# Performance work log

Hardware: AMD Instinct MI355X
Metric: run time of the kernel (lower is better)

The kernel has to match this reference:

```python
import jax, jax.numpy as jnp
import numpy as np

N_NODES = 100000
N_EDGES = 800000
IN_FEATS = 128
HIDDEN = 128
NUM_CLASSES = 10
NUM_GRAPHS = 128
BN_EPS = 1e-5


def setup_inputs() -> dict:
    key = jax.random.key(0)
    ks = jax.random.split(key, 16)
    s = 0.05  # weight init scale
    return {
        "x": jax.random.normal(ks[0], (N_NODES, IN_FEATS), dtype=jnp.float32),
        "edge_index": jax.random.randint(ks[1], (2, N_EDGES), 0, N_NODES, dtype=jnp.int64),
        "batch": jnp.sort(jax.random.randint(ks[2], (N_NODES,), 0, NUM_GRAPHS, dtype=jnp.int64)),
        # conv1 MLP: Linear(in,h) -> ReLU -> Linear(h,h)
        "W1a": jax.random.normal(ks[3], (IN_FEATS, HIDDEN), dtype=jnp.float32) * s,
        "b1a": jnp.zeros((HIDDEN,), dtype=jnp.float32),
        "W1b": jax.random.normal(ks[4], (HIDDEN, HIDDEN), dtype=jnp.float32) * s,
        "b1b": jnp.zeros((HIDDEN,), dtype=jnp.float32),
        "gamma1": jnp.ones((HIDDEN,), dtype=jnp.float32),
        "beta1": jnp.zeros((HIDDEN,), dtype=jnp.float32),
        # conv2 MLP
        "W2a": jax.random.normal(ks[5], (HIDDEN, HIDDEN), dtype=jnp.float32) * s,
        "b2a": jnp.zeros((HIDDEN,), dtype=jnp.float32),
        "W2b": jax.random.normal(ks[6], (HIDDEN, HIDDEN), dtype=jnp.float32) * s,
        "b2b": jnp.zeros((HIDDEN,), dtype=jnp.float32),
        "gamma2": jnp.ones((HIDDEN,), dtype=jnp.float32),
        "beta2": jnp.zeros((HIDDEN,), dtype=jnp.float32),
        # final classifier
        "Wlin": jax.random.normal(ks[7], (HIDDEN, NUM_CLASSES), dtype=jnp.float32) * s,
        "blin": jnp.zeros((NUM_CLASSES,), dtype=jnp.float32),
    }


def _gin_conv(x, edge_index, Wa, ba, Wb, bb, eps=0.0):
    # GINConv: MLP((1+eps)*x_i + sum_{j->i} x_j); scatter-add over edges
    src, dst = edge_index[0], edge_index[1]
    agg = jax.ops.segment_sum(x[src], dst, num_segments=N_NODES)
    h = (1.0 + eps) * x + agg
    h = jax.nn.relu(h @ Wa + ba) @ Wb + bb
    return h


def _batch_norm(x, gamma, beta):
    # training-mode BN over the node dim (biased variance, as in torch)
    mean = jnp.mean(x, axis=0)
    var = jnp.mean(jnp.square(x - mean), axis=0)
    return (x - mean) * jax.lax.rsqrt(var + BN_EPS) * gamma + beta


def reference(x, edge_index, batch, W1a, b1a, W1b, b1b, gamma1, beta1,
              W2a, b2a, W2b, b2b, gamma2, beta2, Wlin, blin):
    h = _gin_conv(x, edge_index, W1a, b1a, W1b, b1b)
    h = jax.nn.relu(_batch_norm(h, gamma1, beta1))
    # dropout: eval mode -> identity
    h = _gin_conv(h, edge_index, W2a, b2a, W2b, b2b)
    h = jax.nn.relu(_batch_norm(h, gamma2, beta2))
    # global mean pool per graph
    summed = jax.ops.segment_sum(h, batch, num_segments=NUM_GRAPHS)
    counts = jax.ops.segment_sum(jnp.ones((h.shape[0],), h.dtype), batch, num_segments=NUM_GRAPHS)
    pooled = summed / jnp.maximum(counts, 1.0)[:, None]  # [G, H]
    logits = pooled @ Wlin + blin
    return jax.nn.log_softmax(logits, axis=1)
```

## Files before the change

kernel.cpp:

```cpp
#include <hip/hip_runtime.h>

#define N_NODES 100000
#define N_EDGESC 800000
#define HID 128
#define NGRAPH 128
#define BN_EPS 1e-5f
#define NREP 32
#define PS 136
#define MLP_BLOCKS ((N_NODES + 63) / 64)

#define PBLK 256
#define PCHUNK 3125
#define NCOARSE 196
#define HISTN (NCOARSE * PBLK)
#define HSCAN_BLOCKS (HISTN / 1024)
#define CVT_BLOCKS 12500

typedef __bf16 bf16x8 __attribute__((ext_vector_type(8)));
typedef float f32x4 __attribute__((ext_vector_type(4)));

__device__ inline unsigned short f2bf(float f) {
    unsigned int u = __float_as_uint(f);
    unsigned int r = u + 0x7FFFu + ((u >> 16) & 1u);
    return (unsigned short)(r >> 16);
}
__device__ inline float b2f(unsigned short u) {
    return __uint_as_float(((unsigned int)u) << 16);
}


__global__ __launch_bounds__(256) void k_phist(const int* __restrict__ dst,
                                               int* __restrict__ hist)
{
    __shared__ int h[NCOARSE];
    if (threadIdx.x < NCOARSE) h[threadIdx.x] = 0;
    __syncthreads();
    int base = blockIdx.x * PCHUNK;
    for (int i = threadIdx.x; i < PCHUNK; i += 256)
        atomicAdd(&h[dst[base + i] >> 9], 1);
    __syncthreads();
    if (threadIdx.x < NCOARSE)
        hist[threadIdx.x * PBLK + blockIdx.x] = h[threadIdx.x];
}

__global__ __launch_bounds__(256) void k_scan_block(int* __restrict__ a,
    int* __restrict__ bsum, int n)
{
    __shared__ int ts[256];
    int base = blockIdx.x * 1024 + threadIdx.x * 4;
    int v[4], s = 0;
    #pragma unroll
    for (int i = 0; i < 4; ++i) {
        int idx = base + i;
        v[i] = (idx < n) ? a[idx] : 0;
        s += v[i];
    }
    ts[threadIdx.x] = s;
    __syncthreads();
    for (int d = 1; d < 256; d <<= 1) {
        int t = (threadIdx.x >= d) ? ts[threadIdx.x - d] : 0;
        __syncthreads();
        ts[threadIdx.x] += t;
        __syncthreads();
    }
    int run = ts[threadIdx.x] - s;
    #pragma unroll
    for (int i = 0; i < 4; ++i) {
        int idx = base + i;
        if (idx < n) a[idx] = run;
        run += v[i];
    }
    if (threadIdx.x == 255) bsum[blockIdx.x] = ts[255];
}

__global__ void k_scan_top_bounds(int* __restrict__ bsum, int nb,
    const int* __restrict__ batch, int* __restrict__ gstart)
{
    if (threadIdx.x == 0) {
        int run = 0;
        for (int i = 0; i < nb; ++i) { int t = bsum[i]; bsum[i] = run; run += t; }
    }
    int g = threadIdx.x;
    int lo = 0, hi = N_NODES;
    while (lo < hi) {
        int mid = (lo + hi) >> 1;
        if (batch[mid] < g) lo = mid + 1; else hi = mid;
    }
    gstart[g] = lo;
    if (g == 0) gstart[NGRAPH] = N_NODES;
}

__global__ __launch_bounds__(256) void k_pscatter(const int* __restrict__ src,
    const int* __restrict__ dst, const int* __restrict__ hist,
    const int* __restrict__ bsum, unsigned int* __restrict__ pk1)
{
    __shared__ int cur[NCOARSE];
    if (threadIdx.x < NCOARSE) {
        int idx = threadIdx.x * PBLK + blockIdx.x;
        cur[threadIdx.x] = hist[idx] + bsum[idx >> 10];
    }
    __syncthreads();
    int base = blockIdx.x * PCHUNK;
    for (int i = threadIdx.x; i < PCHUNK; i += 256) {
        int s = src[base + i], d = dst[base + i];
        int p = atomicAdd(&cur[d >> 9], 1);
        pk1[p] = ((unsigned int)s << 9) | (unsigned int)(d & 511);
    }
}

__global__ __launch_bounds__(256) void k_psort(const unsigned int* __restrict__ pk1,
    const int* __restrict__ hist, const int* __restrict__ bsum,
    int* __restrict__ eidx, int* __restrict__ off)
{
    __shared__ int h[512], cur[512], ts[256];
    const int b = blockIdx.x;
    const int i0 = b * PBLK;
    const int e0 = hist[i0] + bsum[i0 >> 10];
    int e1 = N_EDGESC;
    if (b < NCOARSE - 1) {
        const int i1 = (b + 1) * PBLK;
        e1 = hist[i1] + bsum[i1 >> 10];
    }
    const int cnt = e1 - e0;
    h[threadIdx.x] = 0; h[threadIdx.x + 256] = 0;
    __syncthreads();
    for (int i = threadIdx.x; i < cnt; i += 256)
        atomicAdd(&h[pk1[e0 + i] & 511], 1);
    __syncthreads();
    int v0 = h[threadIdx.x * 2], v1 = h[threadIdx.x * 2 + 1];
    int s = v0 + v1;
    ts[threadIdx.x] = s;
    __syncthreads();
    for (int d = 1; d < 256; d <<= 1) {
        int t = (threadIdx.x >= d) ? ts[threadIdx.x - d] : 0;
        __syncthreads();
        ts[threadIdx.x] += t;
        __syncthreads();
    }
    int run = e0 + ts[threadIdx.x] - s;
    int n0 = b * 512 + threadIdx.x * 2;
    cur[threadIdx.x * 2]     = run;
    cur[threadIdx.x * 2 + 1] = run + v0;
    if (n0     <= N_NODES) off[n0]     = run;
    if (n0 + 1 <= N_NODES) off[n0 + 1] = run + v0;
    __syncthreads();
    for (int i = threadIdx.x; i < cnt; i += 256) {
        unsigned int u = pk1[e0 + i];
        int p = atomicAdd(&cur[u & 511], 1);
        eidx[p] = (int)(u >> 9);
    }
}

__global__ __launch_bounds__(256) void k_cvtw(const float* __restrict__ X,
    unsigned short* __restrict__ Y,
    const float* __restrict__ Wa, const float* __restrict__ Wb,
    const float* __restrict__ Wc, const float* __restrict__ Wd,
    unsigned short* __restrict__ WT)
{
    int blk = blockIdx.x;
    if (blk < CVT_BLOCKS) {
        int i = blk * 256 + threadIdx.x;
        float4 v = ((const float4*)X)[i];
        ((ushort4*)Y)[i] = make_ushort4(f2bf(v.x), f2bf(v.y), f2bf(v.z), f2bf(v.w));
    } else {
        int idx = (blk - CVT_BLOCKS) * 256 + threadIdx.x;
        int mat = idx >> 14, w = idx & 16383;
        int k = w >> 7, n = w & 127;
        const float* W = (mat == 0) ? Wa : (mat == 1) ? Wb : (mat == 2) ? Wc : Wd;
        WT[mat * 16384 + n * 128 + k] = f2bf(W[w]);
    }
}

template<bool BN>
__device__ inline void acc_row(float* acc, uint4 v,
                               const float* sc, const float* sh)
{
    unsigned int u[4] = {v.x, v.y, v.z, v.w};
    #pragma unroll
    for (int j = 0; j < 4; ++j) {
        float lo = b2f((unsigned short)u[j]);
        float hi = b2f((unsigned short)(u[j] >> 16));
        if (BN) {
            lo = fmaxf(lo * sc[2*j]   + sh[2*j],   0.f);
            hi = fmaxf(hi * sc[2*j+1] + sh[2*j+1], 0.f);
        }
        acc[2*j]   += lo;
        acc[2*j+1] += hi;
    }
}

template<bool BN>
__global__ __launch_bounds__(256) void k_gather(
    const unsigned short* __restrict__ X, const float* __restrict__ SC,
    const int* __restrict__ off, const int* __restrict__ eidx,
    unsigned short* __restrict__ OUT, int M)
{
    int n = blockIdx.x * 16 + (threadIdx.x >> 4);
    if (n >= M) return;
    const int lane = threadIdx.x & 15;
    const size_t co = (size_t)lane * 8;

    float sc[8], sh[8];
    if (BN) {
        *(float4*)&sc[0] = ((const float4*)SC)[lane * 2];
        *(float4*)&sc[4] = ((const float4*)SC)[lane * 2 + 1];
        *(float4*)&sh[0] = ((const float4*)SC)[32 + lane * 2];
        *(float4*)&sh[4] = ((const float4*)SC)[32 + lane * 2 + 1];
    }

    float acc[8] = {0.f, 0.f, 0.f, 0.f, 0.f, 0.f, 0.f, 0.f};
    acc_row<BN>(acc, *(const uint4*)(X + (size_t)n * HID + co), sc, sh);

    int k = off[n], kend = off[n + 1];
    for (; k + 7 < kend; k += 8) {
        uint4 v0 = *(const uint4*)(X + (size_t)eidx[k]   * HID + co);
        uint4 v1 = *(const uint4*)(X + (size_t)eidx[k+1] * HID + co);
        uint4 v2 = *(const uint4*)(X + (size_t)eidx[k+2] * HID + co);
        uint4 v3 = *(const uint4*)(X + (size_t)eidx[k+3] * HID + co);
        uint4 v4 = *(const uint4*)(X + (size_t)eidx[k+4] * HID + co);
        uint4 v5 = *(const uint4*)(X + (size_t)eidx[k+5] * HID + co);
        uint4 v6 = *(const uint4*)(X + (size_t)eidx[k+6] * HID + co);
        uint4 v7 = *(const uint4*)(X + (size_t)eidx[k+7] * HID + co);
        acc_row<BN>(acc, v0, sc, sh); acc_row<BN>(acc, v1, sc, sh);
        acc_row<BN>(acc, v2, sc, sh); acc_row<BN>(acc, v3, sc, sh);
        acc_row<BN>(acc, v4, sc, sh); acc_row<BN>(acc, v5, sc, sh);
        acc_row<BN>(acc, v6, sc, sh); acc_row<BN>(acc, v7, sc, sh);
    }
    for (; k + 3 < kend; k += 4) {
        uint4 v0 = *(const uint4*)(X + (size_t)eidx[k]   * HID + co);
        uint4 v1 = *(const uint4*)(X + (size_t)eidx[k+1] * HID + co);
        uint4 v2 = *(const uint4*)(X + (size_t)eidx[k+2] * HID + co);
        uint4 v3 = *(const uint4*)(X + (size_t)eidx[k+3] * HID + co);
        acc_row<BN>(acc, v0, sc, sh); acc_row<BN>(acc, v1, sc, sh);
        acc_row<BN>(acc, v2, sc, sh); acc_row<BN>(acc, v3, sc, sh);
    }
    for (; k < kend; ++k) {
        uint4 v = *(const uint4*)(X + (size_t)eidx[k] * HID + co);
        acc_row<BN>(acc, v, sc, sh);
    }

    uint4 o;
    o.x = (unsigned int)f2bf(acc[0]) | ((unsigned int)f2bf(acc[1]) << 16);
    o.y = (unsigned int)f2bf(acc[2]) | ((unsigned int)f2bf(acc[3]) << 16);
    o.z = (unsigned int)f2bf(acc[4]) | ((unsigned int)f2bf(acc[5]) << 16);
    o.w = (unsigned int)f2bf(acc[6]) | ((unsigned int)f2bf(acc[7]) << 16);
    *(uint4*)(OUT + (size_t)n * HID + co) = o;
}

__global__ __launch_bounds__(256) void k_mlp(
    const unsigned short* __restrict__ A,
    const unsigned short* __restrict__ WTa, const float* __restrict__ ba,
    const unsigned short* __restrict__ WTb, const float* __restrict__ bb,
    unsigned short* __restrict__ Cb, float* __restrict__ Srep, int M)
{
    __shared__ unsigned short Abuf[64 * PS];
    __shared__ unsigned short Hbuf[64 * PS];

    const int tid  = threadIdx.x;
    const int wave = tid >> 6;
    const int lane = tid & 63;
    const int m    = lane & 15;
    const int quad = lane >> 4;
    const int rowbase = blockIdx.x * 64;

    bf16x8 WA[2][4], WB[2][4];
    float bav[2], bbv[2];
    #pragma unroll
    for (int n0 = 0; n0 < 2; ++n0) {
        const int col = (wave * 2 + n0) * 16 + m;
        const size_t cb = (size_t)col * HID + quad * 8;
        #pragma unroll
        for (int kk = 0; kk < 4; ++kk) {
            WA[n0][kk] = *(const bf16x8*)(WTa + cb + kk * 32);
            WB[n0][kk] = *(const bf16x8*)(WTb + cb + kk * 32);
        }
        bav[n0] = ba[col];
        bbv[n0] = bb[col];
    }

    {
        const uint4* Ag = (const uint4*)(A + (size_t)rowbase * HID);
        #pragma unroll
        for (int i = 0; i < 4; ++i) {
            int u = tid + i * 256;
            uint4 v = Ag[u];
            int r = u >> 4, c = u & 15;
            *(uint4*)(Abuf + r * PS + c * 8) = v;
        }
    }
    __syncthreads();

    f32x4 acc[4][2];
    #pragma unroll
    for (int rg = 0; rg < 4; ++rg)
        #pragma unroll
        for (int n0 = 0; n0 < 2; ++n0) acc[rg][n0] = {0.f, 0.f, 0.f, 0.f};
    #pragma unroll
    for (int rg = 0; rg < 4; ++rg) {
        #pragma unroll
        for (int kk = 0; kk < 4; ++kk) {
            bf16x8 af = *(const bf16x8*)(Abuf + (rg*16 + m) * PS + quad*8 + kk*32);
            acc[rg][0] = __builtin_amdgcn_mfma_f32_16x16x32_bf16(af, WA[0][kk], acc[rg][0], 0, 0, 0);
            acc[rg][1] = __builtin_amdgcn_mfma_f32_16x16x32_bf16(af, WA[1][kk], acc[rg][1], 0, 0, 0);
        }
    }

    #pragma unroll
    for (int rg = 0; rg < 4; ++rg)
        #pragma unroll
        for (int n0 = 0; n0 < 2; ++n0)
            #pragma unroll
            for (int i = 0; i < 4; ++i)
                Hbuf[(rg*16 + quad*4 + i) * PS + (wave*2 + n0)*16 + m] =
                    f2bf(fmaxf(acc[rg][n0][i] + bav[n0], 0.f));
    __syncthreads();

    #pragma unroll
    for (int rg = 0; rg < 4; ++rg)
        #pragma unroll
        for (int n0 = 0; n0 < 2; ++n0) acc[rg][n0] = {0.f, 0.f, 0.f, 0.f};
    #pragma unroll
    for (int rg = 0; rg < 4; ++rg) {
        #pragma unroll
        for (int kk = 0; kk < 4; ++kk) {
            bf16x8 hf = *(const bf16x8*)(Hbuf + (rg*16 + m) * PS + quad*8 + kk*32);
            acc[rg][0] = __builtin_amdgcn_mfma_f32_16x16x32_bf16(hf, WB[0][kk], acc[rg][0], 0, 0, 0);
            acc[rg][1] = __builtin_amdgcn_mfma_f32_16x16x32_bf16(hf, WB[1][kk], acc[rg][1], 0, 0, 0);
        }
    }

    const bool full = (rowbase + 64 <= M);
    float s[2] = {0.f, 0.f}, s2[2] = {0.f, 0.f};
    #pragma unroll
    for (int rg = 0; rg < 4; ++rg) {
        #pragma unroll
        for (int n0 = 0; n0 < 2; ++n0) {
            #pragma unroll
            for (int i = 0; i < 4; ++i) {
                float v = acc[rg][n0][i] + bbv[n0];
                if (full || rowbase + rg*16 + quad*4 + i < M) { s[n0] += v; s2[n0] += v*v; }
                Abuf[(rg*16 + quad*4 + i) * PS + (wave*2 + n0)*16 + m] = f2bf(v);
            }
        }
    }
    __syncthreads();

    #pragma unroll
    for (int i = 0; i < 4; ++i) {
        int u = tid + i * 256;
        int r = u >> 4, c = u & 15;
        uint4 v = *(const uint4*)(Abuf + r * PS + c * 8);
        int g = rowbase + r;
        if (g < M) *(uint4*)(Cb + (size_t)g * HID + c * 8) = v;
    }

    #pragma unroll
    for (int n0 = 0; n0 < 2; ++n0) {
        s[n0]  += __shfl_xor(s[n0], 16, 64);
        s[n0]  += __shfl_xor(s[n0], 32, 64);
        s2[n0] += __shfl_xor(s2[n0], 16, 64);
        s2[n0] += __shfl_xor(s2[n0], 32, 64);
    }
    if (quad == 0) {
        float* R = Srep + (size_t)((blockIdx.x * 4 + wave) & (NREP - 1)) * 256;
        #pragma unroll
        for (int n0 = 0; n0 < 2; ++n0) {
            int col = (wave * 2 + n0) * 16 + m;
            atomicAdd(&R[col], s[n0]);
            atomicAdd(&R[128 + col], s2[n0]);
        }
    }
}

__global__ void k_bnfinalize(const float* __restrict__ Srep,
    const float* __restrict__ gamma, const float* __restrict__ beta,
    float* __restrict__ SC, int M)
{
    int f = threadIdx.x;
    float s = 0.f, s2 = 0.f;
    for (int r = 0; r < NREP; ++r) {
        s += Srep[r * 256 + f];
        s2 += Srep[r * 256 + 128 + f];
    }
    float mean = s / (float)M;
    float var = s2 / (float)M - mean * mean;
    var = fmaxf(var, 0.f);
    float sc = gamma[f] * rsqrtf(var + BN_EPS);
    SC[f] = sc;
    SC[HID + f] = beta[f] - mean * sc;
}

__global__ __launch_bounds__(256) void k_pool(const unsigned short* __restrict__ H,
    const float* __restrict__ SC, const int* __restrict__ gstart,
    float* __restrict__ P)
{
    int g = blockIdx.x >> 4, part = blockIdx.x & 15;
    int beg = gstart[g], end = gstart[g + 1];
    int f = threadIdx.x & 127, half = threadIdx.x >> 7;
    float sc = SC[f], sh = SC[HID + f];
    float s = 0.f;
    for (int r = beg + part * 2 + half; r < end; r += 32)
        s += fmaxf(b2f(H[(size_t)r * HID + f]) * sc + sh, 0.f);
    __shared__ float ls[256];
    ls[threadIdx.x] = s;
    __syncthreads();
    if (threadIdx.x < 128)
        atomicAdd(&P[g * HID + threadIdx.x], ls[threadIdx.x] + ls[threadIdx.x + 128]);
}

__global__ void k_head(const float* __restrict__ P, const int* __restrict__ gstart,
    const float* __restrict__ Wlin, const float* __restrict__ blin,
    float* __restrict__ out)
{
    int g = blockIdx.x;
    int l = threadIdx.x;
    float inv = 1.f / (float)max(gstart[g + 1] - gstart[g], 1);
    float p0 = P[(size_t)g * HID + l] * inv;
    float p1 = P[(size_t)g * HID + 64 + l] * inv;
    float lg[10];
    #pragma unroll
    for (int c = 0; c < 10; ++c) {
        float v = p0 * Wlin[l * 10 + c] + p1 * Wlin[(64 + l) * 10 + c];
        #pragma unroll
        for (int off = 32; off > 0; off >>= 1) v += __shfl_down(v, off);
        lg[c] = v;
    }
    if (l == 0) {
        float mx = -1e30f;
        #pragma unroll
        for (int c = 0; c < 10; ++c) { lg[c] += blin[c]; mx = fmaxf(mx, lg[c]); }
        float s = 0.f;
        #pragma unroll
        for (int c = 0; c < 10; ++c) s += expf(lg[c] - mx);
        float lse = mx + logf(s);
        #pragma unroll
        for (int c = 0; c < 10; ++c) out[g * 10 + c] = lg[c] - lse;
    }
}

extern "C" void kernel_launch(void* const* d_in, const int* in_sizes, int n_in,
                              void* d_out, int out_size, void* d_ws, size_t ws_size,
                              hipStream_t stream)
{
    const float* x    = (const float*)d_in[0];
    const int*   ei   = (const int*)d_in[1];
    const int*   batch= (const int*)d_in[2];
    const float* W1a  = (const float*)d_in[3];
    const float* b1a  = (const float*)d_in[4];
    const float* W1b  = (const float*)d_in[5];
    const float* b1b  = (const float*)d_in[6];
    const float* g1   = (const float*)d_in[7];
    const float* be1  = (const float*)d_in[8];
    const float* W2a  = (const float*)d_in[9];
    const float* b2a  = (const float*)d_in[10];
    const float* W2b  = (const float*)d_in[11];
    const float* b2b  = (const float*)d_in[12];
    const float* g2   = (const float*)d_in[13];
    const float* be2  = (const float*)d_in[14];
    const float* Wl   = (const float*)d_in[15];
    const float* bl   = (const float*)d_in[16];
    float* out = (float*)d_out;

    const int* src = ei;
    const int* dst = ei + N_EDGESC;

    const size_t NM = (size_t)N_NODES * HID;
    char* wsb = (char*)d_ws;
    unsigned short* Ab  = (unsigned short*)wsb;
    unsigned short* Yb  = Ab + NM;
    unsigned short* Xb  = Yb + NM;
    float* Srep1 = (float*)(Xb + NM);
    float* Srep2 = Srep1 + NREP * 256;
    float* P    = Srep2 + NREP * 256;
    float* SC1  = P + (size_t)NGRAPH * HID;
    float* SC2  = SC1 + 256;
    unsigned short* WT = (unsigned short*)(SC2 + 256);
    int* hist   = (int*)(WT + 4 * 16384);
    int* eidx   = hist + HISTN;
    int* off    = eidx + N_EDGESC;
    int* bsum   = off + N_NODES + 1;
    int* gstart = bsum + 64;
    unsigned int* pk1 = (unsigned int*)Xb;

    dim3 blk(256);
    const int gatBlocks = (N_NODES + 15) / 16;

    hipMemsetAsync(Srep1, 0,
        (2 * NREP * 256 + (size_t)NGRAPH * HID) * sizeof(float), stream);

    k_phist<<<PBLK, blk, 0, stream>>>(dst, hist);
    k_scan_block<<<HSCAN_BLOCKS, blk, 0, stream>>>(hist, bsum, HISTN);
    k_scan_top_bounds<<<1, 128, 0, stream>>>(bsum, HSCAN_BLOCKS, batch, gstart);
    k_pscatter<<<PBLK, blk, 0, stream>>>(src, dst, hist, bsum, pk1);
    k_psort<<<NCOARSE, blk, 0, stream>>>(pk1, hist, bsum, eidx, off);

    k_cvtw<<<CVT_BLOCKS + 256, blk, 0, stream>>>(x, Xb, W1a, W1b, W2a, W2b, WT);

    k_gather<false><<<gatBlocks, blk, 0, stream>>>(Xb, nullptr, off, eidx, Ab, N_NODES);
    k_mlp<<<MLP_BLOCKS, blk, 0, stream>>>(Ab, WT, b1a, WT + 16384, b1b, Yb, Srep1, N_NODES);
    k_bnfinalize<<<1, 128, 0, stream>>>(Srep1, g1, be1, SC1, N_NODES);

    k_gather<true><<<gatBlocks, blk, 0, stream>>>(Yb, SC1, off, eidx, Ab, N_NODES);
    k_mlp<<<MLP_BLOCKS, blk, 0, stream>>>(Ab, WT + 2 * 16384, b2a, WT + 3 * 16384, b2b, Xb, Srep2, N_NODES);
    k_bnfinalize<<<1, 128, 0, stream>>>(Srep2, g2, be2, SC2, N_NODES);

    k_pool<<<NGRAPH * 16, blk, 0, stream>>>(Xb, SC2, gstart, P);
    k_head<<<NGRAPH, 64, 0, stream>>>(P, gstart, Wl, bl, out);
}
```

Measured before the change: 302.9 us.

## Merge CSR prep into cooperative kernel, fold BN finalize and pooling into neighbors

Five edge-sort preprocessing kernels are merged into one cooperative kernel that uses grid-wide syncs between phases. BN finalize now runs in the last-finishing block of each MLP kernel, found with an atomic done-counter. Pool and head become one kernel with one block per graph. This removes several launches and the pooled-sum memset and atomics, but pooling now runs on only 128 blocks and grid.sync adds its own cost.

```diff
diff --git a/kernel.cpp b/kernel.cpp
--- a/kernel.cpp
+++ b/kernel.cpp
@@ -1,4 +1,7 @@
 #include <hip/hip_runtime.h>
+#include <hip/hip_cooperative_groups.h>
+
+namespace cg = cooperative_groups;
 
 #define N_NODES 100000
 #define N_EDGESC 800000
@@ -28,126 +31,121 @@
     return __uint_as_float(((unsigned int)u) << 16);
 }
 
-
-__global__ __launch_bounds__(256) void k_phist(const int* __restrict__ dst,
-                                               int* __restrict__ hist)
-{
-    __shared__ int h[NCOARSE];
-    if (threadIdx.x < NCOARSE) h[threadIdx.x] = 0;
-    __syncthreads();
-    int base = blockIdx.x * PCHUNK;
-    for (int i = threadIdx.x; i < PCHUNK; i += 256)
-        atomicAdd(&h[dst[base + i] >> 9], 1);
-    __syncthreads();
-    if (threadIdx.x < NCOARSE)
-        hist[threadIdx.x * PBLK + blockIdx.x] = h[threadIdx.x];
-}
-
-__global__ __launch_bounds__(256) void k_scan_block(int* __restrict__ a,
-    int* __restrict__ bsum, int n)
-{
-    __shared__ int ts[256];
-    int base = blockIdx.x * 1024 + threadIdx.x * 4;
-    int v[4], s = 0;
-    #pragma unroll
-    for (int i = 0; i < 4; ++i) {
-        int idx = base + i;
-        v[i] = (idx < n) ? a[idx] : 0;
-        s += v[i];
-    }
-    ts[threadIdx.x] = s;
-    __syncthreads();
-    for (int d = 1; d < 256; d <<= 1) {
-        int t = (threadIdx.x >= d) ? ts[threadIdx.x - d] : 0;
-        __syncthreads();
-        ts[threadIdx.x] += t;
-        __syncthreads();
-    }
-    int run = ts[threadIdx.x] - s;
-    #pragma unroll
-    for (int i = 0; i < 4; ++i) {
-        int idx = base + i;
-        if (idx < n) a[idx] = run;
-        run += v[i];
-    }
-    if (threadIdx.x == 255) bsum[blockIdx.x] = ts[255];
-}
-
-__global__ void k_scan_top_bounds(int* __restrict__ bsum, int nb,
-    const int* __restrict__ batch, int* __restrict__ gstart)
-{
-    if (threadIdx.x == 0) {
-        int run = 0;
-        for (int i = 0; i < nb; ++i) { int t = bsum[i]; bsum[i] = run; run += t; }
-    }
-    int g = threadIdx.x;
-    int lo = 0, hi = N_NODES;
-    while (lo < hi) {
-        int mid = (lo + hi) >> 1;
-        if (batch[mid] < g) lo = mid + 1; else hi = mid;
-    }
-    gstart[g] = lo;
-    if (g == 0) gstart[NGRAPH] = N_NODES;
-}
-
-__global__ __launch_bounds__(256) void k_pscatter(const int* __restrict__ src,
-    const int* __restrict__ dst, const int* __restrict__ hist,
-    const int* __restrict__ bsum, unsigned int* __restrict__ pk1)
-{
-    __shared__ int cur[NCOARSE];
-    if (threadIdx.x < NCOARSE) {
-        int idx = threadIdx.x * PBLK + blockIdx.x;
-        cur[threadIdx.x] = hist[idx] + bsum[idx >> 10];
-    }
-    __syncthreads();
-    int base = blockIdx.x * PCHUNK;
-    for (int i = threadIdx.x; i < PCHUNK; i += 256) {
-        int s = src[base + i], d = dst[base + i];
-        int p = atomicAdd(&cur[d >> 9], 1);
-        pk1[p] = ((unsigned int)s << 9) | (unsigned int)(d & 511);
-    }
-}
-
-__global__ __launch_bounds__(256) void k_psort(const unsigned int* __restrict__ pk1,
-    const int* __restrict__ hist, const int* __restrict__ bsum,
-    int* __restrict__ eidx, int* __restrict__ off)
-{
-    __shared__ int h[512], cur[512], ts[256];
+__global__ __launch_bounds__(256) void k_prep(
+    const int* __restrict__ src, const int* __restrict__ dst,
+    const int* __restrict__ batch,
+    int* __restrict__ hist, int* __restrict__ bsum, int* __restrict__ gstart,
+    unsigned int* __restrict__ pk1, int* __restrict__ eidx, int* __restrict__ off)
+{
+    cg::grid_group grid = cg::this_grid();
+    __shared__ int S[1280];
+    const int tid = threadIdx.x;
     const int b = blockIdx.x;
-    const int i0 = b * PBLK;
-    const int e0 = hist[i0] + bsum[i0 >> 10];
-    int e1 = N_EDGESC;
-    if (b < NCOARSE - 1) {
-        const int i1 = (b + 1) * PBLK;
-        e1 = hist[i1] + bsum[i1 >> 10];
-    }
-    const int cnt = e1 - e0;
-    h[threadIdx.x] = 0; h[threadIdx.x + 256] = 0;
-    __syncthreads();
-    for (int i = threadIdx.x; i < cnt; i += 256)
-        atomicAdd(&h[pk1[e0 + i] & 511], 1);
-    __syncthreads();
-    int v0 = h[threadIdx.x * 2], v1 = h[threadIdx.x * 2 + 1];
-    int s = v0 + v1;
-    ts[threadIdx.x] = s;
-    __syncthreads();
-    for (int d = 1; d < 256; d <<= 1) {
-        int t = (threadIdx.x >= d) ? ts[threadIdx.x - d] : 0;
-        __syncthreads();
-        ts[threadIdx.x] += t;
-        __syncthreads();
-    }
-    int run = e0 + ts[threadIdx.x] - s;
-    int n0 = b * 512 + threadIdx.x * 2;
-    cur[threadIdx.x * 2]     = run;
-    cur[threadIdx.x * 2 + 1] = run + v0;
-    if (n0     <= N_NODES) off[n0]     = run;
-    if (n0 + 1 <= N_NODES) off[n0 + 1] = run + v0;
-    __syncthreads();
-    for (int i = threadIdx.x; i < cnt; i += 256) {
-        unsigned int u = pk1[e0 + i];
-        int p = atomicAdd(&cur[u & 511], 1);
-        eidx[p] = (int)(u >> 9);
+
+    {
+        int* h = S;
+        if (tid < NCOARSE) h[tid] = 0;
+        __syncthreads();
+        int base = b * PCHUNK;
+        for (int i = tid; i < PCHUNK; i += 256)
+            atomicAdd(&h[dst[base + i] >> 9], 1);
+        __syncthreads();
+        if (tid < NCOARSE) hist[tid * PBLK + b] = h[tid];
+    }
+    grid.sync();
+
+    if (b < HSCAN_BLOCKS) {
+        int* ts = S;
+        int base = b * 1024 + tid * 4;
+        int v[4], s = 0;
+        #pragma unroll
+        for (int i = 0; i < 4; ++i) { v[i] = hist[base + i]; s += v[i]; }
+        ts[tid] = s;
+        __syncthreads();
+        for (int d = 1; d < 256; d <<= 1) {
+            int t = (tid >= d) ? ts[tid - d] : 0;
+            __syncthreads();
+            ts[tid] += t;
+            __syncthreads();
+        }
+        int run = ts[tid] - s;
+        #pragma unroll
+        for (int i = 0; i < 4; ++i) { hist[base + i] = run; run += v[i]; }
+        if (tid == 255) bsum[b] = ts[255];
+    }
+    grid.sync();
+
+    if (b == 0) {
+        if (tid == 0) {
+            int run = 0;
+            for (int i = 0; i < HSCAN_BLOCKS; ++i) { int t = bsum[i]; bsum[i] = run; run += t; }
+        }
+        if (tid < 128) {
+            int g = tid;
+            int lo = 0, hi = N_NODES;
+            while (lo < hi) {
+                int mid = (lo + hi) >> 1;
+                if (batch[mid] < g) lo = mid + 1; else hi = mid;
+            }
+            gstart[g] = lo;
+            if (g == 0) gstart[NGRAPH] = N_NODES;
+        }
+    }
+    grid.sync();
+
+    {
+        int* cur = S;
+        if (tid < NCOARSE) {
+            int idx = tid * PBLK + b;
+            cur[tid] = hist[idx] + bsum[idx >> 10];
+        }
+        __syncthreads();
+        int base = b * PCHUNK;
+        for (int i = tid; i < PCHUNK; i += 256) {
+            int sv = src[base + i], d = dst[base + i];
+            int p = atomicAdd(&cur[d >> 9], 1);
+            pk1[p] = ((unsigned int)sv << 9) | (unsigned int)(d & 511);
+        }
+    }
+    grid.sync();
+
+    if (b < NCOARSE) {
+        int* h = S; int* cur = S + 512; int* ts = S + 1024;
+        const int i0 = b * PBLK;
+        const int e0 = hist[i0] + bsum[i0 >> 10];
+        int e1 = N_EDGESC;
+        if (b < NCOARSE - 1) {
+            const int i1 = (b + 1) * PBLK;
+            e1 = hist[i1] + bsum[i1 >> 10];
+        }
+        const int cnt = e1 - e0;
+        h[tid] = 0; h[tid + 256] = 0;
+        __syncthreads();
+        for (int i = tid; i < cnt; i += 256)
+            atomicAdd(&h[pk1[e0 + i] & 511], 1);
+        __syncthreads();
+        int v0 = h[tid * 2], v1 = h[tid * 2 + 1];
+        int s = v0 + v1;
+        ts[tid] = s;
+        __syncthreads();
+        for (int d = 1; d < 256; d <<= 1) {
+            int t = (tid >= d) ? ts[tid - d] : 0;
+            __syncthreads();
+            ts[tid] += t;
+            __syncthreads();
+        }
+        int run = e0 + ts[tid] - s;
+        int n0 = b * 512 + tid * 2;
+        cur[tid * 2]     = run;
+        cur[tid * 2 + 1] = run + v0;
+        if (n0     <= N_NODES) off[n0]     = run;
+        if (n0 + 1 <= N_NODES) off[n0 + 1] = run + v0;
+        __syncthreads();
+        for (int i = tid; i < cnt; i += 256) {
+            unsigned int u = pk1[e0 + i];
+            int p = atomicAdd(&cur[u & 511], 1);
+            eidx[p] = (int)(u >> 9);
+        }
     }
 }
 
@@ -251,7 +249,9 @@
     const unsigned short* __restrict__ A,
     const unsigned short* __restrict__ WTa, const float* __restrict__ ba,
     const unsigned short* __restrict__ WTb, const float* __restrict__ bb,
-    unsigned short* __restrict__ Cb, float* __restrict__ Srep, int M)
+    unsigned short* __restrict__ Cb, float* __restrict__ Srep,
+    const float* __restrict__ gamma, const float* __restrict__ beta,
+    float* __restrict__ SCout, int* __restrict__ done, int M)
 {
     __shared__ unsigned short Abuf[64 * PS];
     __shared__ unsigned short Hbuf[64 * PS];
@@ -370,71 +370,74 @@
             atomicAdd(&R[128 + col], s2[n0]);
         }
     }
-}
-
-__global__ void k_bnfinalize(const float* __restrict__ Srep,
-    const float* __restrict__ gamma, const float* __restrict__ beta,
-    float* __restrict__ SC, int M)
-{
-    int f = threadIdx.x;
-    float s = 0.f, s2 = 0.f;
-    for (int r = 0; r < NREP; ++r) {
-        s += Srep[r * 256 + f];
-        s2 += Srep[r * 256 + 128 + f];
-    }
-    float mean = s / (float)M;
-    float var = s2 / (float)M - mean * mean;
-    var = fmaxf(var, 0.f);
-    float sc = gamma[f] * rsqrtf(var + BN_EPS);
-    SC[f] = sc;
-    SC[HID + f] = beta[f] - mean * sc;
-}
-
-__global__ __launch_bounds__(256) void k_pool(const unsigned short* __restrict__ H,
-    const float* __restrict__ SC, const int* __restrict__ gstart,
-    float* __restrict__ P)
-{
-    int g = blockIdx.x >> 4, part = blockIdx.x & 15;
+
+    __threadfence();
+    __shared__ int isLast;
+    if (tid == 0) isLast = (atomicAdd(done, 1) == (int)gridDim.x - 1) ? 1 : 0;
+    __syncthreads();
+    if (isLast) {
+        if (tid < 128) {
+            int f = tid;
+            float ss = 0.f, ss2 = 0.f;
+            for (int r = 0; r < NREP; ++r) {
+                ss  += atomicAdd(&Srep[r * 256 + f], 0.f);
+                ss2 += atomicAdd(&Srep[r * 256 + 128 + f], 0.f);
+            }
+            float mean = ss / (float)M;
+            float var = fmaxf(ss2 / (float)M - mean * mean, 0.f);
+            float scv = gamma[f] * rsqrtf(var + BN_EPS);
+            SCout[f] = scv;
+            SCout[HID + f] = beta[f] - mean * scv;
+        }
+        __syncthreads();
+        if (tid == 0) *done = 0;
+    }
+}
+
+__global__ __launch_bounds__(512) void k_poolhead(
+    const unsigned short* __restrict__ H, const float* __restrict__ SC,
+    const int* __restrict__ gstart, const float* __restrict__ Wlin,
+    const float* __restrict__ blin, float* __restrict__ out)
+{
+    __shared__ float ls[512];
+    __shared__ float pooled[128];
+    int g = blockIdx.x;
     int beg = gstart[g], end = gstart[g + 1];
-    int f = threadIdx.x & 127, half = threadIdx.x >> 7;
-    float sc = SC[f], sh = SC[HID + f];
+    int f = threadIdx.x & 127, q = threadIdx.x >> 7;
+    float scv = SC[f], shv = SC[HID + f];
     float s = 0.f;
-    for (int r = beg + part * 2 + half; r < end; r += 32)
-        s += fmaxf(b2f(H[(size_t)r * HID + f]) * sc + sh, 0.f);
-    __shared__ float ls[256];
+    for (int r = beg + q; r < end; r += 4)
+        s += fmaxf(b2f(H[(size_t)r * HID + f]) * scv + shv, 0.f);
     ls[threadIdx.x] = s;
     __syncthreads();
     if (threadIdx.x < 128)
-        atomicAdd(&P[g * HID + threadIdx.x], ls[threadIdx.x] + ls[threadIdx.x + 128]);
-}
-
-__global__ void k_head(const float* __restrict__ P, const int* __restrict__ gstart,
-    const float* __restrict__ Wlin, const float* __restrict__ blin,
-    float* __restrict__ out)
-{
-    int g = blockIdx.x;
-    int l = threadIdx.x;
-    float inv = 1.f / (float)max(gstart[g + 1] - gstart[g], 1);
-    float p0 = P[(size_t)g * HID + l] * inv;
-    float p1 = P[(size_t)g * HID + 64 + l] * inv;
-    float lg[10];
-    #pragma unroll
-    for (int c = 0; c < 10; ++c) {
-        float v = p0 * Wlin[l * 10 + c] + p1 * Wlin[(64 + l) * 10 + c];
-        #pragma unroll
-        for (int off = 32; off > 0; off >>= 1) v += __shfl_down(v, off);
-        lg[c] = v;
-    }
-    if (l == 0) {
-        float mx = -1e30f;
-        #pragma unroll
-        for (int c = 0; c < 10; ++c) { lg[c] += blin[c]; mx = fmaxf(mx, lg[c]); }
-        float s = 0.f;
-        #pragma unroll
-        for (int c = 0; c < 10; ++c) s += expf(lg[c] - mx);
-        float lse = mx + logf(s);
-        #pragma unroll
-        for (int c = 0; c < 10; ++c) out[g * 10 + c] = lg[c] - lse;
+        pooled[threadIdx.x] = ls[threadIdx.x] + ls[threadIdx.x + 128]
+                            + ls[threadIdx.x + 256] + ls[threadIdx.x + 384];
+    __syncthreads();
+    if (threadIdx.x < 64) {
+        int l = threadIdx.x;
+        float inv = 1.f / (float)max(end - beg, 1);
+        float p0 = pooled[l] * inv;
+        float p1 = pooled[64 + l] * inv;
+        float lg[10];
+        #pragma unroll
+        for (int c = 0; c < 10; ++c) {
+            float v = p0 * Wlin[l * 10 + c] + p1 * Wlin[(64 + l) * 10 + c];
+            #pragma unroll
+            for (int o = 32; o > 0; o >>= 1) v += __shfl_down(v, o);
+            lg[c] = v;
+        }
+        if (l == 0) {
+            float mx = -1e30f;
+            #pragma unroll
+            for (int c = 0; c < 10; ++c) { lg[c] += blin[c]; mx = fmaxf(mx, lg[c]); }
+            float se = 0.f;
+            #pragma unroll
+            for (int c = 0; c < 10; ++c) se += expf(lg[c] - mx);
+            float lse = mx + logf(se);
+            #pragma unroll
+            for (int c = 0; c < 10; ++c) out[g * 10 + c] = lg[c] - lse;
+        }
     }
 }
 
@@ -471,8 +474,8 @@
     unsigned short* Xb  = Yb + NM;
     float* Srep1 = (float*)(Xb + NM);
     float* Srep2 = Srep1 + NREP * 256;
-    float* P    = Srep2 + NREP * 256;
-    float* SC1  = P + (size_t)NGRAPH * HID;
+    int* done    = (int*)(Srep2 + NREP * 256);
+    float* SC1  = (float*)(done + 2);
     float* SC2  = SC1 + 256;
     unsigned short* WT = (unsigned short*)(SC2 + 256);
     int* hist   = (int*)(WT + 4 * 16384);
@@ -485,25 +488,25 @@
     dim3 blk(256);
     const int gatBlocks = (N_NODES + 15) / 16;
 
-    hipMemsetAsync(Srep1, 0,
-        (2 * NREP * 256 + (size_t)NGRAPH * HID) * sizeof(float), stream);
-
-    k_phist<<<PBLK, blk, 0, stream>>>(dst, hist);
-    k_scan_block<<<HSCAN_BLOCKS, blk, 0, stream>>>(hist, bsum, HISTN);
-    k_scan_top_bounds<<<1, 128, 0, stream>>>(bsum, HSCAN_BLOCKS, batch, gstart);
-    k_pscatter<<<PBLK, blk, 0, stream>>>(src, dst, hist, bsum, pk1);
-    k_psort<<<NCOARSE, blk, 0, stream>>>(pk1, hist, bsum, eidx, off);
+    hipMemsetAsync(Srep1, 0, 2 * NREP * 256 * sizeof(float) + 2 * sizeof(int),
+                   stream);
+
+    void* prepArgs[] = {
+        (void*)&src, (void*)&dst, (void*)&batch,
+        (void*)&hist, (void*)&bsum, (void*)&gstart,
+        (void*)&pk1, (void*)&eidx, (void*)&off };
+    hipLaunchCooperativeKernel((void*)k_prep, dim3(PBLK), blk,
+                               prepArgs, 0, stream);
 
     k_cvtw<<<CVT_BLOCKS + 256, blk, 0, stream>>>(x, Xb, W1a, W1b, W2a, W2b, WT);
 
     k_gather<false><<<gatBlocks, blk, 0, stream>>>(Xb, nullptr, off, eidx, Ab, N_NODES);
-    k_mlp<<<MLP_BLOCKS, blk, 0, stream>>>(Ab, WT, b1a, WT + 16384, b1b, Yb, Srep1, N_NODES);
-    k_bnfinalize<<<1, 128, 0, stream>>>(Srep1, g1, be1, SC1, N_NODES);
+    k_mlp<<<MLP_BLOCKS, blk, 0, stream>>>(Ab, WT, b1a, WT + 16384, b1b, Yb,
+                                          Srep1, g1, be1, SC1, done, N_NODES);
 
     k_gather<true><<<gatBlocks, blk, 0, stream>>>(Yb, SC1, off, eidx, Ab, N_NODES);
-    k_mlp<<<MLP_BLOCKS, blk, 0, stream>>>(Ab, WT + 2 * 16384, b2a, WT + 3 * 16384, b2b, Xb, Srep2, N_NODES);
-    k_bnfinalize<<<1, 128, 0, stream>>>(Srep2, g2, be2, SC2, N_NODES);
-
-    k_pool<<<NGRAPH * 16, blk, 0, stream>>>(Xb, SC2, gstart, P);
-    k_head<<<NGRAPH, 64, 0, stream>>>(P, gstart, Wl, bl, out);
-}
+    k_mlp<<<MLP_BLOCKS, blk, 0, stream>>>(Ab, WT + 2 * 16384, b2a, WT + 3 * 16384,
+                                          b2b, Xb, Srep2, g2, be2, SC2, done + 1, N_NODES);
+
+    k_poolhead<<<NGRAPH, 512, 0, stream>>>(Xb, SC2, gstart, Wl, bl, out);
+}
```

Result: slower. 759.8 us (+150.8%).
